# Kernel tuning notes

Hardware: AMD Instinct MI355X
Metric: run time of the kernel (lower is better)

## Reference

```python
import jax, jax.numpy as jnp
import numpy as np

C = 256
GROUPS = 32
EPS = 1e-5


def setup_inputs() -> dict:
    key = jax.random.key(0)
    ks = jax.random.split(key, 6)
    b, c, H, W = 8, C, 64, 64
    s = 1.0 / np.sqrt(c)
    return {
        "x": jax.random.normal(ks[0], (b, c, H, W), dtype=jnp.float32),
        "gn_scale": jnp.ones((c,), jnp.float32),
        "gn_bias": jnp.zeros((c,), jnp.float32),
        "wq": jax.random.normal(ks[1], (c, c), jnp.float32) * s,
        "bq": jnp.zeros((c,), jnp.float32),
        "wk": jax.random.normal(ks[2], (c, c), jnp.float32) * s,
        "bk": jnp.zeros((c,), jnp.float32),
        "wv": jax.random.normal(ks[3], (c, c), jnp.float32) * s,
        "bv": jnp.zeros((c,), jnp.float32),
        "wo": jax.random.normal(ks[4], (c, c), jnp.float32) * s,
        "bo": jnp.zeros((c,), jnp.float32),
    }


def reference(x, gn_scale, gn_bias, wq, bq, wk, bk, wv, bv, wo, bo):
    b, c, H, W = x.shape
    N = H * W
    # GroupNorm(32, c)
    xg = x.reshape(b, GROUPS, c // GROUPS, H, W)
    mean = xg.mean(axis=(2, 3, 4), keepdims=True)
    var = xg.var(axis=(2, 3, 4), keepdims=True)
    xn = ((xg - mean) * jax.lax.rsqrt(var + EPS)).reshape(b, c, H, W)
    xn = xn * gn_scale[None, :, None, None] + gn_bias[None, :, None, None]
    xf = xn.reshape(b, c, N)  # [b, c, N]
    # 1x1 convs == per-pixel channel matmuls
    q = jnp.einsum('oc,bcn->bon', wq, xf) + bq[None, :, None]
    k = jnp.einsum('oc,bcn->bon', wk, xf) + bk[None, :, None]
    v = jnp.einsum('oc,bcn->bon', wv, xf) + bv[None, :, None]
    # attention: scores [b, N, N]
    scale = 1.0 / jnp.sqrt(jnp.asarray(c, x.dtype))
    w = jnp.einsum('bcn,bcm->bnm', q, k) * scale
    w = jax.nn.softmax(w, axis=-1)
    attn = jnp.einsum('bnm,bcm->bcn', w, v)  # [b, c, N]
    out = jnp.einsum('oc,bcn->bon', wo, attn) + bo[None, :, None]
    return x + out.reshape(b, c, H, W)
```

## Files before the change

kernel.cpp:

```cpp
#include <hip/hip_runtime.h>

typedef __attribute__((ext_vector_type(8))) short short8;
typedef __attribute__((ext_vector_type(4))) float floatx4;
typedef __attribute__((ext_vector_type(16))) float floatx16;
typedef __attribute__((ext_vector_type(4))) int intx4;

#define NPIX 4096
#define CH 256

static __device__ __forceinline__ unsigned short f2bf(float f) {
  union { float f; unsigned int u; } v; v.f = f;
  unsigned int u = v.u;
  return (unsigned short)((u + 0x7FFFu + ((u >> 16) & 1u)) >> 16);
}

static __device__ __forceinline__ unsigned int pk2bf(float a, float b) {
  union { float f; unsigned int u; } x, y; x.f = a; y.f = b;
  return __builtin_amdgcn_perm(y.u + 0x8000u, x.u + 0x8000u, 0x07060302u);
}

typedef __attribute__((address_space(3))) unsigned int lds_uint;
typedef const __attribute__((address_space(1))) unsigned int glob_uint;
static __device__ __forceinline__ void gload16(const void* g, void* l) {
  __builtin_amdgcn_global_load_lds((glob_uint*)g, (lds_uint*)l, 16, 0, 0);
}

__global__ void conv_weights_kernel(const float* __restrict__ wq, const float* __restrict__ wk,
                                    const float* __restrict__ wv, const float* __restrict__ wo,
                                    unsigned short* __restrict__ wqkv, unsigned short* __restrict__ wob) {
  int i = blockIdx.x * 256 + threadIdx.x;
  wqkv[i]          = f2bf(wq[i]);
  wqkv[65536 + i]  = f2bf(wk[i]);
  wqkv[131072 + i] = f2bf(wv[i]);
  wob[i]           = f2bf(wo[i]);
}

__global__ __launch_bounds__(256) void gn_kernel(const float* __restrict__ x,
                                                 const float* __restrict__ gsc,
                                                 const float* __restrict__ gbi,
                                                 unsigned short* __restrict__ xnT) {
  int blk = blockIdx.x; int b = blk >> 5; int g = blk & 31;
  int c0 = g * 8;
  const float* xb = x + ((size_t)b * CH + c0) * NPIX;
  int tid = threadIdx.x;
  float s = 0.f, ss = 0.f;
#pragma unroll
  for (int ci = 0; ci < 8; ++ci) {
    const floatx4* p = (const floatx4*)(xb + (size_t)ci * NPIX);
    for (int n4 = tid; n4 < 1024; n4 += 256) {
      floatx4 v = p[n4];
      s += v[0] + v[1] + v[2] + v[3];
      ss += v[0]*v[0] + v[1]*v[1] + v[2]*v[2] + v[3]*v[3];
    }
  }
#pragma unroll
  for (int o = 32; o > 0; o >>= 1) { s += __shfl_down(s, o); ss += __shfl_down(ss, o); }
  __shared__ float red[10];
  int wid = tid >> 6;
  if ((tid & 63) == 0) { red[wid] = s; red[4 + wid] = ss; }
  __syncthreads();
  if (tid == 0) {
    float S = red[0] + red[1] + red[2] + red[3];
    float SS = red[4] + red[5] + red[6] + red[7];
    float mean = S * (1.f / 32768.f);
    float var = SS * (1.f / 32768.f) - mean * mean;
    red[8] = mean; red[9] = rsqrtf(var + 1e-5f);
  }
  __syncthreads();
  float mean = red[8], rstd = red[9];
  float sc[8], bi[8];
#pragma unroll
  for (int ci = 0; ci < 8; ++ci) {
    float scale = gsc[c0 + ci] * rstd;
    sc[ci] = scale;
    bi[ci] = gbi[c0 + ci] - mean * scale;
  }
  for (int n4 = tid; n4 < 1024; n4 += 256) {
    floatx4 v[8];
#pragma unroll
    for (int ci = 0; ci < 8; ++ci) v[ci] = ((const floatx4*)(xb + (size_t)ci * NPIX))[n4];
#pragma unroll
    for (int j = 0; j < 4; ++j) {
      alignas(16) unsigned short tmp[8];
#pragma unroll
      for (int ci = 0; ci < 8; ++ci) tmp[ci] = f2bf(v[ci][j] * sc[ci] + bi[ci]);
      *(intx4*)(xnT + ((size_t)(b * NPIX + n4 * 4 + j)) * CH + c0) = *(const intx4*)tmp;
    }
  }
}

__global__ __launch_bounds__(256, 2) void qkv_gemm(
    const unsigned short* __restrict__ wqkv, const unsigned short* __restrict__ xnT,
    const float* __restrict__ bq, const float* __restrict__ bk, const float* __restrict__ bv,
    unsigned short* __restrict__ qT, unsigned short* __restrict__ kT, unsigned short* __restrict__ vC) {
  int nt = blockIdx.x, ot = blockIdx.y, bz = blockIdx.z;
  int which = bz % 3, b = bz / 3;
  const unsigned short* W = wqkv + which * 65536;
  const float* bias = which == 0 ? bq : (which == 1 ? bk : bv);
  const unsigned short* X = xnT + (size_t)b * NPIX * CH;
  int o0 = ot * 128, n0 = nt * 128;

  __shared__ unsigned short As[128 * 64];
  __shared__ unsigned short Bs[128 * 64];

  int tid = threadIdx.x;
  int wave = tid >> 6, lane = tid & 63, quad = lane >> 4, l16 = lane & 15;
  int wm = (wave >> 1) * 64, wn = (wave & 1) * 64;

  floatx4 acc[4][4];
#pragma unroll
  for (int i = 0; i < 4; ++i)
#pragma unroll
    for (int j = 0; j < 4; ++j) acc[i][j] = (floatx4){0.f, 0.f, 0.f, 0.f};

  for (int k0 = 0; k0 < 256; k0 += 64) {
    __syncthreads();
#pragma unroll
    for (int c2 = 0; c2 < 4; ++c2) {
      int row = wave * 32 + c2 * 8 + (lane >> 3);
      int sc = (lane & 7) ^ (row & 7);
      gload16(W + (size_t)(o0 + row) * CH + k0 + sc * 8, &As[(wave * 32 + c2 * 8) * 64]);
      gload16(X + (size_t)(n0 + row) * CH + k0 + sc * 8, &Bs[(wave * 32 + c2 * 8) * 64]);
    }
    __syncthreads();
#pragma unroll
    for (int s = 0; s < 2; ++s) {
      short8 af[4], bf[4];
#pragma unroll
      for (int i = 0; i < 4; ++i) {
        int m = wm + i * 16 + l16;
        af[i] = *(const short8*)(As + m * 64 + (((s * 4 + quad) ^ (m & 7)) * 8));
        int n = wn + i * 16 + l16;
        bf[i] = *(const short8*)(Bs + n * 64 + (((s * 4 + quad) ^ (n & 7)) * 8));
      }
#pragma unroll
      for (int i = 0; i < 4; ++i)
#pragma unroll
        for (int j = 0; j < 4; ++j)
          acc[i][j] = __builtin_amdgcn_mfma_f32_16x16x32_bf16(af[i], bf[j], acc[i][j], 0, 0, 0);
    }
  }

  if (which < 2) {
    float qs = (which == 0) ? 0.090168440f : 1.0f;
    unsigned short* outp = (which == 0 ? qT : kT) + (size_t)b * NPIX * CH;
#pragma unroll
    for (int i = 0; i < 4; ++i) {
      int obase = o0 + wm + i * 16 + quad * 4;
      float bias4[4];
#pragma unroll
      for (int r = 0; r < 4; ++r) bias4[r] = bias[obase + r];
#pragma unroll
      for (int j = 0; j < 4; ++j) {
        int n = n0 + wn + j * 16 + l16;
        uint2 pk;
        pk.x = pk2bf((acc[i][j][0] + bias4[0]) * qs, (acc[i][j][1] + bias4[1]) * qs);
        pk.y = pk2bf((acc[i][j][2] + bias4[2]) * qs, (acc[i][j][3] + bias4[3]) * qs);
        *(uint2*)(outp + (size_t)n * CH + obase) = pk;
      }
    }
  } else {
    unsigned short* outp = vC + (size_t)b * CH * NPIX;
#pragma unroll
    for (int i = 0; i < 4; ++i)
#pragma unroll
      for (int r = 0; r < 4; ++r) {
        int o = o0 + wm + i * 16 + quad * 4 + r;
        float bb = bias[o];
#pragma unroll
        for (int j = 0; j < 4; ++j) {
          int n = n0 + wn + j * 16 + l16;
          outp[(size_t)o * NPIX + n] = f2bf(acc[i][j][r] + bb);
        }
      }
  }
}

__global__ __launch_bounds__(512, 2) void attn_kernel(
    const unsigned short* __restrict__ qT, const unsigned short* __restrict__ kT,
    const unsigned short* __restrict__ vC, unsigned short* __restrict__ aT) {
  __shared__ unsigned short Klds[2][64 * 256];
  __shared__ unsigned short Vlds[2][256 * 64];
  __shared__ unsigned short Plds[128 * 64];
  __shared__ float lred[128][2];

  const int tid = threadIdx.x;
  const int w = tid >> 6, lane = tid & 63;
  const int l32 = lane & 31, h = lane >> 5;
  const int b = blockIdx.x & 7, qt = blockIdx.x >> 3;
  const int qbase = qt * 128;

  const unsigned short* Kb = kT + (size_t)b * NPIX * CH;
  const unsigned short* Vb = vC + (size_t)b * CH * NPIX;

  const int msl = (w & 1) * 32, qsl = (w >> 1) * 32;
  const int csl = (w & 3) * 64, qh = (w >> 2) * 64;

  short8 qf[16];
  {
    const unsigned short* qp = qT + ((size_t)(b * NPIX + qbase + qsl + l32)) * CH + h * 8;
#pragma unroll
    for (int s = 0; s < 16; ++s) qf[s] = *(const short8*)(qp + s * 16);
  }

  floatx16 oacc[2][2] = {};
  float l_acc = 0.f;

#define STAGE(KT)                                                                         \
  {                                                                                       \
    int m0_ = (KT) * 64;                                                                  \
    int bb_ = (KT) & 1;                                                                   \
    if (w < 4) {                                                                          \
      _Pragma("unroll") for (int j = 0; j < 8; ++j) {                                     \
        int r0 = w * 16 + j * 2 + (lane >> 5);                                            \
        gload16(Kb + (size_t)(m0_ + r0) * CH + (((lane & 31) ^ (r0 & 7)) * 8),            \
                &Klds[bb_][(w * 16 + j * 2) * 256]);                                      \
      }                                                                                   \
    } else {                                                                              \
      _Pragma("unroll") for (int j = 0; j < 8; ++j) {                                     \
        int c_ = (w - 4) * 64 + j * 8 + (lane >> 3);                                      \
        gload16(Vb + (size_t)c_ * NPIX + m0_ + (((lane & 7) ^ (c_ & 7)) * 8),             \
                &Vlds[bb_][((w - 4) * 64 + j * 8) * 64]);                                 \
      }                                                                                   \
    }                                                                                     \
  }

  STAGE(0);

  for (int kt = 0; kt < 64; ++kt) {
    const int buf = kt & 1;
    asm volatile("s_waitcnt vmcnt(0) lgkmcnt(0)\ns_barrier" ::: "memory");
    if (kt + 1 < 64) STAGE(kt + 1);

    floatx16 sacc = {};
    {
      const int m = msl + l32;
      const unsigned short* kr = &Klds[buf][m * 256];
      const int mx = m & 7;
#pragma unroll
      for (int s = 0; s < 16; ++s) {
        short8 kf = *(const short8*)(kr + (((s * 2 + h) ^ mx) * 8));
        sacc = __builtin_amdgcn_mfma_f32_32x32x16_bf16(kf, qf[s], sacc, 0, 0, 0);
      }
    }
    float sum = 0.f;
#pragma unroll
    for (int r = 0; r < 16; ++r) {
      float p = exp2f(sacc[r]);
      sacc[r] = p; sum += p;
    }
    sum += __shfl_xor(sum, 32);
    l_acc += sum;

    {
      int qrow = qsl + l32;
#pragma unroll
      for (int t = 0; t < 4; ++t) {
        int phys = ((msl >> 3) + t) ^ (qrow & 7);
        uint2 wv;
        wv.x = pk2bf(sacc[4 * t], sacc[4 * t + 1]);
        wv.y = pk2bf(sacc[4 * t + 2], sacc[4 * t + 3]);
        *(uint2*)&Plds[qrow * 64 + phys * 8 + h * 4] = wv;
      }
    }
    asm volatile("s_waitcnt lgkmcnt(0)\ns_barrier" ::: "memory");

#pragma unroll
    for (int mstep = 0; mstep < 4; ++mstep) {
      short8 pf[2], vf[2];
#pragma unroll
      for (int qsub = 0; qsub < 2; ++qsub) {
        int q = qh + qsub * 32 + l32;
        pf[qsub] = *(const short8*)&Plds[q * 64 + (((mstep * 2 + h) ^ (q & 7)) * 8)];
      }
#pragma unroll
      for (int csub = 0; csub < 2; ++csub) {
        int c = csl + csub * 32 + l32;
        vf[csub] = *(const short8*)&Vlds[buf][c * 64 + (((mstep * 2 + h) ^ (c & 7)) * 8)];
      }
#pragma unroll
      for (int csub = 0; csub < 2; ++csub)
#pragma unroll
        for (int qsub = 0; qsub < 2; ++qsub)
          oacc[csub][qsub] =
              __builtin_amdgcn_mfma_f32_32x32x16_bf16(vf[csub], pf[qsub], oacc[csub][qsub], 0, 0, 0);
    }
  }
#undef STAGE

  if (lane < 32) lred[qsl + l32][w & 1] = l_acc;
  __syncthreads();
  float inv[2];
#pragma unroll
  for (int qsub = 0; qsub < 2; ++qsub) {
    int q = qh + qsub * 32 + l32;
    inv[qsub] = 1.f / (lred[q][0] + lred[q][1]);
  }
  unsigned short* ab = aT + (size_t)b * NPIX * CH;
#pragma unroll
  for (int csub = 0; csub < 2; ++csub)
#pragma unroll
    for (int qsub = 0; qsub < 2; ++qsub) {
      int qg = qbase + qh + qsub * 32 + l32;
      float iv = inv[qsub];
#pragma unroll
      for (int t = 0; t < 4; ++t) {
        int c = csl + csub * 32 + 8 * t + 4 * h;
        uint2 wv;
        wv.x = pk2bf(oacc[csub][qsub][4 * t] * iv, oacc[csub][qsub][4 * t + 1] * iv);
        wv.y = pk2bf(oacc[csub][qsub][4 * t + 2] * iv, oacc[csub][qsub][4 * t + 3] * iv);
        *(uint2*)(ab + (size_t)qg * CH + c) = wv;
      }
    }
}

__global__ __launch_bounds__(256, 2) void out_gemm(
    const unsigned short* __restrict__ wob, const unsigned short* __restrict__ aT,
    const float* __restrict__ bo, const float* __restrict__ x, float* __restrict__ outp) {
  int nt = blockIdx.x, ot = blockIdx.y, b = blockIdx.z;
  const unsigned short* A = aT + (size_t)b * NPIX * CH;
  int o0 = ot * 128, n0 = nt * 128;

  __shared__ unsigned short As[128 * 64];
  __shared__ unsigned short Bs[128 * 64];

  int tid = threadIdx.x;
  int wave = tid >> 6, lane = tid & 63, quad = lane >> 4, l16 = lane & 15;
  int wm = (wave >> 1) * 64, wn = (wave & 1) * 64;

  floatx4 acc[4][4];
#pragma unroll
  for (int i = 0; i < 4; ++i)
#pragma unroll
    for (int j = 0; j < 4; ++j) acc[i][j] = (floatx4){0.f, 0.f, 0.f, 0.f};

  for (int k0 = 0; k0 < 256; k0 += 64) {
    __syncthreads();
#pragma unroll
    for (int c2 = 0; c2 < 4; ++c2) {
      int row = wave * 32 + c2 * 8 + (lane >> 3);
      int sc = (lane & 7) ^ (row & 7);
      gload16(wob + (size_t)(o0 + row) * CH + k0 + sc * 8, &As[(wave * 32 + c2 * 8) * 64]);
      gload16(A + (size_t)(n0 + row) * CH + k0 + sc * 8, &Bs[(wave * 32 + c2 * 8) * 64]);
    }
    __syncthreads();
#pragma unroll
    for (int s = 0; s < 2; ++s) {
      short8 af[4], bf[4];
#pragma unroll
      for (int i = 0; i < 4; ++i) {
        int m = wm + i * 16 + l16;
        af[i] = *(const short8*)(As + m * 64 + (((s * 4 + quad) ^ (m & 7)) * 8));
        int n = wn + i * 16 + l16;
        bf[i] = *(const short8*)(Bs + n * 64 + (((s * 4 + quad) ^ (n & 7)) * 8));
      }
#pragma unroll
      for (int i = 0; i < 4; ++i)
#pragma unroll
        for (int j = 0; j < 4; ++j)
          acc[i][j] = __builtin_amdgcn_mfma_f32_16x16x32_bf16(af[i], bf[j], acc[i][j], 0, 0, 0);
    }
  }

#pragma unroll
  for (int i = 0; i < 4; ++i)
#pragma unroll
    for (int r = 0; r < 4; ++r) {
      int o = o0 + wm + i * 16 + quad * 4 + r;
      float bb = bo[o];
#pragma unroll
      for (int j = 0; j < 4; ++j) {
        int n = n0 + wn + j * 16 + l16;
        size_t idx = ((size_t)b * CH + o) * NPIX + n;
        outp[idx] = x[idx] + bb + acc[i][j][r];
      }
    }
}

extern "C" void kernel_launch(void* const* d_in, const int* in_sizes, int n_in,
                              void* d_out, int out_size, void* d_ws, size_t ws_size,
                              hipStream_t stream) {
  const float* x   = (const float*)d_in[0];
  const float* gsc = (const float*)d_in[1];
  const float* gbi = (const float*)d_in[2];
  const float* wq  = (const float*)d_in[3];
  const float* bq  = (const float*)d_in[4];
  const float* wk  = (const float*)d_in[5];
  const float* bk  = (const float*)d_in[6];
  const float* wv  = (const float*)d_in[7];
  const float* bv  = (const float*)d_in[8];
  const float* wo  = (const float*)d_in[9];
  const float* bo  = (const float*)d_in[10];
  float* out = (float*)d_out;

  char* ws = (char*)d_ws;
  unsigned short* xnT  = (unsigned short*)(ws);
  unsigned short* qT   = (unsigned short*)(ws + 16777216);
  unsigned short* kT   = (unsigned short*)(ws + 33554432);
  unsigned short* vC   = (unsigned short*)(ws + 50331648);
  unsigned short* wqkv = (unsigned short*)(ws + 67108864);
  unsigned short* wob  = (unsigned short*)(ws + 67502080);
  unsigned short* aT   = (unsigned short*)(ws + 67633152);

  conv_weights_kernel<<<256, 256, 0, stream>>>(wq, wk, wv, wo, wqkv, wob);
  gn_kernel<<<256, 256, 0, stream>>>(x, gsc, gbi, xnT);
  dim3 g1(32, 2, 24);
  qkv_gemm<<<g1, 256, 0, stream>>>(wqkv, xnT, bq, bk, bv, qT, kT, vC);
  attn_kernel<<<256, 512, 0, stream>>>(qT, kT, vC, aT);
  dim3 g3(32, 2, 8);
  out_gemm<<<g3, 256, 0, stream>>>(wob, aT, bo, x, out);
}
```

Measured before the change: 315.7 us.

## Enlarge attention key tile to 128 with single-buffered K/V and split staging

The attention kernel now processes 128 keys per iteration instead of 64, so there are 32 iterations and half as many barriers. Each wave computes two 32x32 score tiles that share one K fragment, which reuses K reads from LDS. The double-buffered K/V stage is replaced by single buffers: V for the current tile loads during the QK step, and K for the next tile loads during the PV step. This trades some overlap and more live registers (two Q fragment sets, two score tiles) for fewer barriers and more data reuse; occupancy may drop.

```diff
diff --git a/kernel.cpp b/kernel.cpp
--- a/kernel.cpp
+++ b/kernel.cpp
@@ -179,10 +179,9 @@
 __global__ __launch_bounds__(512, 2) void attn_kernel(
     const unsigned short* __restrict__ qT, const unsigned short* __restrict__ kT,
     const unsigned short* __restrict__ vC, unsigned short* __restrict__ aT) {
-  __shared__ unsigned short Klds[2][64 * 256];
-  __shared__ unsigned short Vlds[2][256 * 64];
-  __shared__ unsigned short Plds[128 * 64];
-  __shared__ float lred[128][2];
+  __shared__ unsigned short Klds[128 * 256];
+  __shared__ unsigned short Vlds[256 * 128];
+  __shared__ unsigned short Plds[128 * 128];
 
   const int tid = threadIdx.x;
   const int w = tid >> 6, lane = tid & 63;
@@ -193,122 +192,136 @@
   const unsigned short* Kb = kT + (size_t)b * NPIX * CH;
   const unsigned short* Vb = vC + (size_t)b * CH * NPIX;
 
-  const int msl = (w & 1) * 32, qsl = (w >> 1) * 32;
-  const int csl = (w & 3) * 64, qh = (w >> 2) * 64;
-
-  short8 qf[16];
+  const int ms  = (w & 3) * 32;
+  const int qp  = (w >> 2) * 64;
+  const int csl = (w & 3) * 64;
+
+  short8 qf[2][16];
   {
-    const unsigned short* qp = qT + ((size_t)(b * NPIX + qbase + qsl + l32)) * CH + h * 8;
-#pragma unroll
-    for (int s = 0; s < 16; ++s) qf[s] = *(const short8*)(qp + s * 16);
-  }
-
-  floatx16 oacc[2][2] = {};
-  float l_acc = 0.f;
-
-#define STAGE(KT)                                                                         \
-  {                                                                                       \
-    int m0_ = (KT) * 64;                                                                  \
-    int bb_ = (KT) & 1;                                                                   \
-    if (w < 4) {                                                                          \
-      _Pragma("unroll") for (int j = 0; j < 8; ++j) {                                     \
-        int r0 = w * 16 + j * 2 + (lane >> 5);                                            \
-        gload16(Kb + (size_t)(m0_ + r0) * CH + (((lane & 31) ^ (r0 & 7)) * 8),            \
-                &Klds[bb_][(w * 16 + j * 2) * 256]);                                      \
-      }                                                                                   \
-    } else {                                                                              \
-      _Pragma("unroll") for (int j = 0; j < 8; ++j) {                                     \
-        int c_ = (w - 4) * 64 + j * 8 + (lane >> 3);                                      \
-        gload16(Vb + (size_t)c_ * NPIX + m0_ + (((lane & 7) ^ (c_ & 7)) * 8),             \
-                &Vlds[bb_][((w - 4) * 64 + j * 8) * 64]);                                 \
-      }                                                                                   \
-    }                                                                                     \
-  }
-
-  STAGE(0);
-
-  for (int kt = 0; kt < 64; ++kt) {
-    const int buf = kt & 1;
+    const unsigned short* qq = qT + ((size_t)(b * NPIX + qbase + qp + l32)) * CH + h * 8;
+#pragma unroll
+    for (int sub = 0; sub < 2; ++sub)
+#pragma unroll
+      for (int ks = 0; ks < 16; ++ks)
+        qf[sub][ks] = *(const short8*)(qq + sub * 32 * CH + ks * 16);
+  }
+
+  floatx16 o00 = {}, o01 = {}, o10 = {}, o11 = {};
+  float l0 = 0.f, l1 = 0.f;
+
+#define STAGE_K(KT)                                                              \
+  {                                                                              \
+    int m0_ = (KT) * 128;                                                        \
+    _Pragma("unroll") for (int j = 0; j < 8; ++j) {                              \
+      int r_ = w * 16 + j * 2 + h;                                               \
+      gload16(Kb + (size_t)(m0_ + r_) * CH + ((l32 ^ (r_ & 7)) * 8),             \
+              &Klds[(w * 16 + j * 2) * 256]);                                    \
+    }                                                                            \
+  }
+#define STAGE_V(KT)                                                              \
+  {                                                                              \
+    int m0_ = (KT) * 128;                                                        \
+    _Pragma("unroll") for (int j = 0; j < 8; ++j) {                              \
+      int c_ = w * 32 + j * 4 + (lane >> 4);                                     \
+      gload16(Vb + (size_t)c_ * NPIX + m0_ + (((lane & 15) ^ (c_ & 7)) * 8),     \
+              &Vlds[(w * 32 + j * 4) * 128]);                                    \
+    }                                                                            \
+  }
+
+  STAGE_K(0);
+  asm volatile("s_waitcnt vmcnt(0)\ns_barrier" ::: "memory");
+
+  for (int kt = 0; kt < 32; ++kt) {
+    STAGE_V(kt);
+
+    floatx16 s0 = {}, s1 = {};
+    {
+      const unsigned short* kr = &Klds[(ms + l32) * 256];
+      const int mx = (ms + l32) & 7;
+#pragma unroll
+      for (int ks = 0; ks < 16; ++ks) {
+        short8 kf = *(const short8*)(kr + (((ks * 2 + h) ^ mx) * 8));
+        s0 = __builtin_amdgcn_mfma_f32_32x32x16_bf16(kf, qf[0][ks], s0, 0, 0, 0);
+        s1 = __builtin_amdgcn_mfma_f32_32x32x16_bf16(kf, qf[1][ks], s1, 0, 0, 0);
+      }
+    }
+    float sum0 = 0.f, sum1 = 0.f;
+#pragma unroll
+    for (int r = 0; r < 16; ++r) {
+      float p0 = exp2f(s0[r]); s0[r] = p0; sum0 += p0;
+      float p1 = exp2f(s1[r]); s1[r] = p1; sum1 += p1;
+    }
+    sum0 += __shfl_xor(sum0, 32); sum1 += __shfl_xor(sum1, 32);
+    l0 += sum0; l1 += sum1;
+
+    {
+      int q0 = qp + l32, q1 = qp + 32 + l32;
+#pragma unroll
+      for (int t = 0; t < 4; ++t) {
+        int g_ = (w & 3) * 4 + t;
+        uint2 wv;
+        wv.x = pk2bf(s0[4 * t], s0[4 * t + 1]);
+        wv.y = pk2bf(s0[4 * t + 2], s0[4 * t + 3]);
+        *(uint2*)((char*)Plds + q0 * 256 + ((g_ ^ (q0 & 7)) * 16) + h * 8) = wv;
+        wv.x = pk2bf(s1[4 * t], s1[4 * t + 1]);
+        wv.y = pk2bf(s1[4 * t + 2], s1[4 * t + 3]);
+        *(uint2*)((char*)Plds + q1 * 256 + ((g_ ^ (q1 & 7)) * 16) + h * 8) = wv;
+      }
+    }
     asm volatile("s_waitcnt vmcnt(0) lgkmcnt(0)\ns_barrier" ::: "memory");
-    if (kt + 1 < 64) STAGE(kt + 1);
-
-    floatx16 sacc = {};
+    if (kt + 1 < 32) STAGE_K(kt + 1);
+
     {
-      const int m = msl + l32;
-      const unsigned short* kr = &Klds[buf][m * 256];
-      const int mx = m & 7;
-#pragma unroll
-      for (int s = 0; s < 16; ++s) {
-        short8 kf = *(const short8*)(kr + (((s * 2 + h) ^ mx) * 8));
-        sacc = __builtin_amdgcn_mfma_f32_32x32x16_bf16(kf, qf[s], sacc, 0, 0, 0);
-      }
-    }
-    float sum = 0.f;
-#pragma unroll
-    for (int r = 0; r < 16; ++r) {
-      float p = exp2f(sacc[r]);
-      sacc[r] = p; sum += p;
-    }
-    sum += __shfl_xor(sum, 32);
-    l_acc += sum;
-
-    {
-      int qrow = qsl + l32;
-#pragma unroll
-      for (int t = 0; t < 4; ++t) {
-        int phys = ((msl >> 3) + t) ^ (qrow & 7);
-        uint2 wv;
-        wv.x = pk2bf(sacc[4 * t], sacc[4 * t + 1]);
-        wv.y = pk2bf(sacc[4 * t + 2], sacc[4 * t + 3]);
-        *(uint2*)&Plds[qrow * 64 + phys * 8 + h * 4] = wv;
-      }
-    }
-    asm volatile("s_waitcnt lgkmcnt(0)\ns_barrier" ::: "memory");
-
-#pragma unroll
-    for (int mstep = 0; mstep < 4; ++mstep) {
-      short8 pf[2], vf[2];
-#pragma unroll
-      for (int qsub = 0; qsub < 2; ++qsub) {
-        int q = qh + qsub * 32 + l32;
-        pf[qsub] = *(const short8*)&Plds[q * 64 + (((mstep * 2 + h) ^ (q & 7)) * 8)];
-      }
-#pragma unroll
-      for (int csub = 0; csub < 2; ++csub) {
-        int c = csl + csub * 32 + l32;
-        vf[csub] = *(const short8*)&Vlds[buf][c * 64 + (((mstep * 2 + h) ^ (c & 7)) * 8)];
-      }
-#pragma unroll
-      for (int csub = 0; csub < 2; ++csub)
-#pragma unroll
-        for (int qsub = 0; qsub < 2; ++qsub)
-          oacc[csub][qsub] =
-              __builtin_amdgcn_mfma_f32_32x32x16_bf16(vf[csub], pf[qsub], oacc[csub][qsub], 0, 0, 0);
-    }
-  }
-#undef STAGE
-
-  if (lane < 32) lred[qsl + l32][w & 1] = l_acc;
+      const int q0 = qp + l32, q1 = qp + 32 + l32;
+      const int c0 = csl + l32, c1 = csl + 32 + l32;
+      const char* Pb = (const char*)Plds;
+      const char* Vl = (const char*)Vlds;
+#pragma unroll
+      for (int ks = 0; ks < 8; ++ks) {
+        int sl = ks * 2 + h;
+        short8 pf0 = *(const short8*)(Pb + q0 * 256 + ((sl ^ (q0 & 7)) * 16));
+        short8 pf1 = *(const short8*)(Pb + q1 * 256 + ((sl ^ (q1 & 7)) * 16));
+        short8 vf0 = *(const short8*)(Vl + c0 * 256 + ((sl ^ (c0 & 7)) * 16));
+        short8 vf1 = *(const short8*)(Vl + c1 * 256 + ((sl ^ (c1 & 7)) * 16));
+        o00 = __builtin_amdgcn_mfma_f32_32x32x16_bf16(vf0, pf0, o00, 0, 0, 0);
+        o01 = __builtin_amdgcn_mfma_f32_32x32x16_bf16(vf0, pf1, o01, 0, 0, 0);
+        o10 = __builtin_amdgcn_mfma_f32_32x32x16_bf16(vf1, pf0, o10, 0, 0, 0);
+        o11 = __builtin_amdgcn_mfma_f32_32x32x16_bf16(vf1, pf1, o11, 0, 0, 0);
+      }
+    }
+    asm volatile("s_waitcnt vmcnt(0) lgkmcnt(0)\ns_barrier" ::: "memory");
+  }
+#undef STAGE_K
+#undef STAGE_V
+
+  float* lred = (float*)Plds;
+  if (lane < 32) {
+    lred[(qp + l32) * 4 + (w & 3)] = l0;
+    lred[(qp + 32 + l32) * 4 + (w & 3)] = l1;
+  }
   __syncthreads();
-  float inv[2];
-#pragma unroll
-  for (int qsub = 0; qsub < 2; ++qsub) {
-    int q = qh + qsub * 32 + l32;
-    inv[qsub] = 1.f / (lred[q][0] + lred[q][1]);
-  }
+  float inv0, inv1;
+  {
+    const float* lp0 = &lred[(qp + l32) * 4];
+    inv0 = 1.f / (lp0[0] + lp0[1] + lp0[2] + lp0[3]);
+    const float* lp1 = &lred[(qp + 32 + l32) * 4];
+    inv1 = 1.f / (lp1[0] + lp1[1] + lp1[2] + lp1[3]);
+  }
+
   unsigned short* ab = aT + (size_t)b * NPIX * CH;
+  const floatx16 oa[2][2] = {{o00, o01}, {o10, o11}};
 #pragma unroll
   for (int csub = 0; csub < 2; ++csub)
 #pragma unroll
     for (int qsub = 0; qsub < 2; ++qsub) {
-      int qg = qbase + qh + qsub * 32 + l32;
-      float iv = inv[qsub];
+      int qg = qbase + qp + qsub * 32 + l32;
+      float iv = qsub ? inv1 : inv0;
 #pragma unroll
       for (int t = 0; t < 4; ++t) {
         int c = csl + csub * 32 + 8 * t + 4 * h;
         uint2 wv;
-        wv.x = pk2bf(oacc[csub][qsub][4 * t] * iv, oacc[csub][qsub][4 * t + 1] * iv);
-        wv.y = pk2bf(oacc[csub][qsub][4 * t + 2] * iv, oacc[csub][qsub][4 * t + 3] * iv);
+        wv.x = pk2bf(oa[csub][qsub][4 * t] * iv, oa[csub][qsub][4 * t + 1] * iv);
+        wv.y = pk2bf(oa[csub][qsub][4 * t + 2] * iv, oa[csub][qsub][4 * t + 3] * iv);
         *(uint2*)(ab + (size_t)qg * CH + c) = wv;
       }
     }
```

Measured after the change: 518.9 us. +64.4%, slower.
